# Kernel tuning notes

Hardware: AMD Instinct MI355X
Metric: run time of the kernel (lower is better)

Reference implementation:

```python
import jax, jax.numpy as jnp
import numpy as np

EPS = 1e-5
K = 20


def knn_idx(x, k):
    # x: (B, N, C) -> (B, N, k) indices of k nearest neighbors (incl. self)
    x2 = jnp.sum(x * x, axis=-1)                         # (B, N)
    inner = jnp.einsum('bnc,bmc->bnm', x, x)             # (B, N, N)
    neg_dist = 2.0 * inner - x2[:, :, None] - x2[:, None, :]
    _, idx = jax.lax.top_k(neg_dist, k)                  # (B, N, k)
    return idx


def graph_feature(x, idx):
    # x: (B, N, C), idx: (B, N, k) -> (B, N, k, 2C) = cat([x_j - x_i, x_i])
    nbr = jax.vmap(lambda xb, ib: xb[ib])(x, idx)        # (B, N, k, C)
    xi = jnp.broadcast_to(x[:, :, None, :], nbr.shape)
    return jnp.concatenate([nbr - xi, xi], axis=-1)


def bn_lrelu(x, gamma, beta):
    # eval-mode BatchNorm (running_mean=0, running_var=1) + LeakyReLU(0.2)
    y = x * (gamma / jnp.sqrt(1.0 + EPS)) + beta
    return jnp.where(y >= 0, y, 0.2 * y)


def edge_conv(x, W, gamma, beta, k):
    # x: (B, N, C) -> (B, N, O); 1x1 conv over edge features + max over k
    idx = knn_idx(x, k)
    feat = graph_feature(x, idx)                         # (B, N, k, 2C)
    y = jnp.einsum('bnkc,oc->bnko', feat, W)
    y = bn_lrelu(y, gamma, beta)
    return jnp.max(y, axis=2)                            # (B, N, O)


def setup_inputs() -> dict:
    key = jax.random.key(0)
    ks = jax.random.split(key, 7)
    d = {
        'points': jax.random.normal(ks[0], (8, 2048, 3), dtype=jnp.float32),
        'W1': jax.random.normal(ks[1], (64, 6), dtype=jnp.float32) * 0.1,
        'W2': jax.random.normal(ks[2], (64, 128), dtype=jnp.float32) * 0.1,
        'W3': jax.random.normal(ks[3], (128, 128), dtype=jnp.float32) * 0.1,
        'W4': jax.random.normal(ks[4], (256, 256), dtype=jnp.float32) * 0.1,
        'W5': jax.random.normal(ks[5], (1024, 512), dtype=jnp.float32) * 0.1,
    }
    for name, c in [('1', 64), ('2', 64), ('3', 128), ('4', 256), ('5', 1024)]:
        d['g' + name] = jnp.ones((c,), dtype=jnp.float32)
        d['b' + name] = jnp.zeros((c,), dtype=jnp.float32)
    return d


def reference(points, W1, W2, W3, W4, W5, g1, g2, g3, g4, g5, b1, b2, b3, b4, b5):
    x1 = edge_conv(points, W1, g1, b1, K)                # (B, N, 64)
    x2 = edge_conv(x1, W2, g2, b2, K)                    # (B, N, 64)
    x3 = edge_conv(x2, W3, g3, b3, K)                    # (B, N, 128)
    x4 = edge_conv(x3, W4, g4, b4, K)                    # (B, N, 256)
    x_cat = jnp.concatenate([x1, x2, x3, x4], axis=-1)   # (B, N, 512)
    feat = bn_lrelu(jnp.einsum('bnc,oc->bno', x_cat, W5), g5, b5)  # (B, N, 1024)
    max_pool = jnp.max(feat, axis=1)
    avg_pool = jnp.mean(feat, axis=1)
    return jnp.concatenate([max_pool, avg_pool], axis=-1)  # (B, 2048)
```

## Files before the change

### kernel.cpp

```cpp
#include <hip/hip_runtime.h>
#include <math.h>

#define BATCH 8
#define NPTS 2048
#define KNN 20
#define BN_TOTAL (BATCH * NPTS)
#define EPSV 1e-5f

__global__ __launch_bounds__(256) void x2_kernel(const float* __restrict__ x, int C, int ldx,
                                                 float* __restrict__ x2) {
    int i = blockIdx.x * 256 + threadIdx.x;
    if (i >= BN_TOTAL) return;
    const float* xr = x + (size_t)i * ldx;
    float s = 0.f;
    if ((ldx & 3) == 0 && (C & 3) == 0) {
        const float4* xr4 = (const float4*)xr;
        for (int c = 0; c < (C >> 2); ++c) {
            float4 v = xr4[c];
            s = fmaf(v.x, v.x, s); s = fmaf(v.y, v.y, s);
            s = fmaf(v.z, v.z, s); s = fmaf(v.w, v.w, s);
        }
    } else {
        for (int c = 0; c < C; ++c) s = fmaf(xr[c], xr[c], s);
    }
    x2[i] = s;
}

__global__ __launch_bounds__(256) void dist_kernel(const float* __restrict__ x,
                                                   const float* __restrict__ x2,
                                                   int C, int ldx, int b0,
                                                   float* __restrict__ S) {
    __shared__ float As[16][136];
    __shared__ float Bs[16][136];
    int z = blockIdx.z;
    int b = b0 + z;
    int i0 = blockIdx.x * 128, j0 = blockIdx.y * 128;
    const float* xb = x + (size_t)b * NPTS * ldx;
    int tid = threadIdx.x;
    int tm = tid >> 4, tn = tid & 15;

    float acc[8][8] = {};
    int KT = (C + 15) >> 4;
    for (int kt = 0; kt < KT; ++kt) {
        int k0 = kt << 4;
#pragma unroll
        for (int s = tid; s < 512; s += 256) {
            int r = s >> 2, c4 = s & 3;
            int kk = k0 + c4 * 4;
            float va[4], vb[4];
            if (kk + 3 < C && (ldx & 3) == 0) {
                float4 a = *(const float4*)&xb[(size_t)(i0 + r) * ldx + kk];
                float4 bv = *(const float4*)&xb[(size_t)(j0 + r) * ldx + kk];
                va[0] = a.x; va[1] = a.y; va[2] = a.z; va[3] = a.w;
                vb[0] = bv.x; vb[1] = bv.y; vb[2] = bv.z; vb[3] = bv.w;
            } else {
#pragma unroll
                for (int u = 0; u < 4; ++u) {
                    int k = kk + u;
                    va[u] = (k < C) ? xb[(size_t)(i0 + r) * ldx + k] : 0.f;
                    vb[u] = (k < C) ? xb[(size_t)(j0 + r) * ldx + k] : 0.f;
                }
            }
#pragma unroll
            for (int u = 0; u < 4; ++u) {
                As[c4 * 4 + u][r] = va[u];
                Bs[c4 * 4 + u][r] = vb[u];
            }
        }
        __syncthreads();
#pragma unroll
        for (int k = 0; k < 16; ++k) {
            float4 a0 = *(const float4*)&As[k][tm * 8];
            float4 a1 = *(const float4*)&As[k][tm * 8 + 4];
            float4 c0 = *(const float4*)&Bs[k][tn * 8];
            float4 c1 = *(const float4*)&Bs[k][tn * 8 + 4];
            float av[8] = {a0.x, a0.y, a0.z, a0.w, a1.x, a1.y, a1.z, a1.w};
            float bv[8] = {c0.x, c0.y, c0.z, c0.w, c1.x, c1.y, c1.z, c1.w};
#pragma unroll
            for (int mi = 0; mi < 8; ++mi)
#pragma unroll
                for (int ni = 0; ni < 8; ++ni)
                    acc[mi][ni] = fmaf(av[mi], bv[ni], acc[mi][ni]);
        }
        __syncthreads();
    }

    const float* x2b = x2 + (size_t)b * NPTS;
    float xj[8];
#pragma unroll
    for (int u = 0; u < 8; ++u) xj[u] = x2b[j0 + tn * 8 + u];
#pragma unroll
    for (int mi = 0; mi < 8; ++mi) {
        float xi = x2b[i0 + tm * 8 + mi];
        float4 o0, o1;
        o0.x = 2.f * acc[mi][0] - xi - xj[0];
        o0.y = 2.f * acc[mi][1] - xi - xj[1];
        o0.z = 2.f * acc[mi][2] - xi - xj[2];
        o0.w = 2.f * acc[mi][3] - xi - xj[3];
        o1.x = 2.f * acc[mi][4] - xi - xj[4];
        o1.y = 2.f * acc[mi][5] - xi - xj[5];
        o1.z = 2.f * acc[mi][6] - xi - xj[6];
        o1.w = 2.f * acc[mi][7] - xi - xj[7];
        size_t rowp = ((size_t)z * NPTS + i0 + tm * 8 + mi) * NPTS + j0 + tn * 8;
        *(float4*)&S[rowp] = o0;
        *(float4*)&S[rowp + 4] = o1;
    }
}

__global__ __launch_bounds__(256) void topk_kernel(const float* __restrict__ S, int b0,
                                                   int* __restrict__ idx_out) {
    int lane = threadIdx.x & 63, w = threadIdx.x >> 6;
    int row = blockIdx.x * 4 + w;
    const float4* S4 = (const float4*)(S + (size_t)row * NPTS);

    float v[32];
    float lm = -INFINITY; int li = 0;
#pragma unroll
    for (int r4 = 0; r4 < 8; ++r4) {
        float4 f = S4[lane * 8 + r4];
        v[r4 * 4 + 0] = f.x; v[r4 * 4 + 1] = f.y;
        v[r4 * 4 + 2] = f.z; v[r4 * 4 + 3] = f.w;
    }
#pragma unroll
    for (int q = 0; q < 32; ++q)
        if (v[q] > lm) { lm = v[q]; li = q; }

    int sel = 0;
    for (int it = 0; it < KNN; ++it) {
        float bv = lm;
        int bi = (lane << 5) | li;
#pragma unroll
        for (int d = 1; d < 64; d <<= 1) {
            float ov = __shfl_xor(bv, d);
            int oi = __shfl_xor(bi, d);
            if (ov > bv || (ov == bv && oi < bi)) { bv = ov; bi = oi; }
        }
        if (lane == it) sel = bi;
        if ((bi >> 5) == lane) {
            int r = bi & 31;
#pragma unroll
            for (int q = 0; q < 32; ++q)
                if (q == r) v[q] = -INFINITY;
            lm = -INFINITY; li = 0;
#pragma unroll
            for (int q = 0; q < 32; ++q)
                if (v[q] > lm) { lm = v[q]; li = q; }
        }
    }
    int z = row >> 11, i = row & 2047;
    int bn = (b0 + z) * NPTS + i;
    if (lane < KNN) idx_out[bn * KNN + lane] = sel;
}

__global__ __launch_bounds__(256) void pq_gemm(const float* __restrict__ X, int C, int ldx,
                                               const float* __restrict__ W, int O,
                                               float* __restrict__ PQ) {
    __shared__ float As[32][68];
    __shared__ float Bs[32][68];
    int i0 = blockIdx.x * 64, j0 = blockIdx.y * 64;
    int tid = threadIdx.x;
    int tm = tid >> 4, tn = tid & 15;
    int N2 = 2 * O;

    float acc[4][4] = {};
    int KT = (C + 31) >> 5;
    for (int kt = 0; kt < KT; ++kt) {
        int k0 = kt << 5;
        for (int e = tid; e < 2048; e += 256) {
            int m = e >> 5, k = e & 31;
            int kk = k0 + k;
            As[k][m] = (kk < C) ? X[(size_t)(i0 + m) * ldx + kk] : 0.f;
            int o = j0 + m;
            float wv = 0.f;
            if (kk < C)
                wv = (o < O) ? W[(size_t)o * 2 * C + kk] : W[(size_t)(o - O) * 2 * C + C + kk];
            Bs[k][m] = wv;
        }
        __syncthreads();
#pragma unroll
        for (int k = 0; k < 32; ++k) {
            float4 a = *(const float4*)&As[k][tm * 4];
            float4 bb = *(const float4*)&Bs[k][tn * 4];
            float av[4] = {a.x, a.y, a.z, a.w};
            float bv[4] = {bb.x, bb.y, bb.z, bb.w};
#pragma unroll
            for (int mi = 0; mi < 4; ++mi)
#pragma unroll
                for (int ni = 0; ni < 4; ++ni)
                    acc[mi][ni] = fmaf(av[mi], bv[ni], acc[mi][ni]);
        }
        __syncthreads();
    }
#pragma unroll
    for (int mi = 0; mi < 4; ++mi) {
        float4 o;
        o.x = acc[mi][0]; o.y = acc[mi][1]; o.z = acc[mi][2]; o.w = acc[mi][3];
        *(float4*)&PQ[(size_t)(i0 + tm * 4 + mi) * N2 + j0 + tn * 4] = o;
    }
}

__global__ __launch_bounds__(256) void gmax_kernel(const float* __restrict__ PQ,
                                                   const int* __restrict__ idx, int O, int oshift,
                                                   const float* __restrict__ gamma,
                                                   const float* __restrict__ beta,
                                                   float* __restrict__ out, int ldo) {
    __shared__ int s_idx[4][KNN];
    int rpb = 256 >> oshift;
    int lr = threadIdx.x >> oshift;
    int o = threadIdx.x & (O - 1);
    int bn = blockIdx.x * rpb + lr;
    int b = bn >> 11;
    if (o < KNN) s_idx[lr][o] = idx[bn * KNN + o];
    __syncthreads();
    const float inv = 1.0f / sqrtf(1.0f + EPSV);
    int N2 = 2 * O;
    size_t brow = (size_t)(b << 11);
    float mx = -INFINITY, mn = INFINITY;
#pragma unroll
    for (int k = 0; k < KNN; ++k) {
        float v = PQ[(brow + s_idx[lr][k]) * N2 + o];
        mx = fmaxf(mx, v);
        mn = fminf(mn, v);
    }
    float pn = PQ[(size_t)bn * N2 + o];
    float qn = PQ[(size_t)bn * N2 + O + o];
    float sc = gamma[o] * inv;
    float m = (sc >= 0.f) ? mx : mn;
    float z = sc * (m - pn + qn) + beta[o];
    out[(size_t)bn * ldo + o] = (z >= 0.f) ? z : 0.2f * z;
}

__global__ __launch_bounds__(256) void final_gemm(const float* __restrict__ xcat,
                                                  const float* __restrict__ W5,
                                                  const float* __restrict__ g5,
                                                  const float* __restrict__ b5,
                                                  float* __restrict__ part) {
    __shared__ float As[16][136];
    __shared__ float Bs[16][136];
    __shared__ float s_red[2][16][132];
    int i0 = blockIdx.x * 128;
    int j0 = blockIdx.y * 128;
    int tid = threadIdx.x;
    int tm = tid >> 4, tn = tid & 15;

    float acc[8][8] = {};
    for (int kt = 0; kt < 32; ++kt) {
        int k0 = kt << 4;
#pragma unroll
        for (int s = tid; s < 512; s += 256) {
            int r = s >> 2, c4 = s & 3;
            int kk = k0 + c4 * 4;
            float4 va = *(const float4*)&xcat[(size_t)(i0 + r) * 512 + kk];
            float4 vb = *(const float4*)&W5[(size_t)(j0 + r) * 512 + kk];
            As[c4 * 4 + 0][r] = va.x; As[c4 * 4 + 1][r] = va.y;
            As[c4 * 4 + 2][r] = va.z; As[c4 * 4 + 3][r] = va.w;
            Bs[c4 * 4 + 0][r] = vb.x; Bs[c4 * 4 + 1][r] = vb.y;
            Bs[c4 * 4 + 2][r] = vb.z; Bs[c4 * 4 + 3][r] = vb.w;
        }
        __syncthreads();
#pragma unroll
        for (int k = 0; k < 16; ++k) {
            float4 a0 = *(const float4*)&As[k][tm * 8];
            float4 a1 = *(const float4*)&As[k][tm * 8 + 4];
            float4 c0 = *(const float4*)&Bs[k][tn * 8];
            float4 c1 = *(const float4*)&Bs[k][tn * 8 + 4];
            float av[8] = {a0.x, a0.y, a0.z, a0.w, a1.x, a1.y, a1.z, a1.w};
            float bv[8] = {c0.x, c0.y, c0.z, c0.w, c1.x, c1.y, c1.z, c1.w};
#pragma unroll
            for (int mi = 0; mi < 8; ++mi)
#pragma unroll
                for (int ni = 0; ni < 8; ++ni)
                    acc[mi][ni] = fmaf(av[mi], bv[ni], acc[mi][ni]);
        }
        __syncthreads();
    }

    const float inv = 1.0f / sqrtf(1.0f + EPSV);
#pragma unroll
    for (int u = 0; u < 8; ++u) {
        int o = j0 + tn * 8 + u;
        float sc = g5[o] * inv;
        float bi = b5[o];
        float mx = -INFINITY, sm = 0.f;
#pragma unroll
        for (int mi = 0; mi < 8; ++mi) {
            float z = fmaf(sc, acc[mi][u], bi);
            z = (z >= 0.f) ? z : 0.2f * z;
            mx = fmaxf(mx, z);
            sm += z;
        }
        s_red[0][tm][tn * 8 + u] = mx;
        s_red[1][tm][tn * 8 + u] = sm;
    }
    __syncthreads();
    if (tid < 128) {
        int o = tid;
        float m = -INFINITY, s = 0.f;
#pragma unroll
        for (int t = 0; t < 16; ++t) {
            m = fmaxf(m, s_red[0][t][o]);
            s += s_red[1][t][o];
        }
        int b = i0 >> 11, nt = (i0 >> 7) & 15;
        size_t base = (size_t)((b * 16 + nt) * 2) * 1024 + j0 + o;
        part[base] = m;
        part[base + 1024] = s;
    }
}

__global__ __launch_bounds__(256) void freduce_kernel(const float* __restrict__ part,
                                                      float* __restrict__ out) {
    int t = blockIdx.x * 256 + threadIdx.x;
    if (t >= 8 * 1024) return;
    int b = t >> 10, o = t & 1023;
    float m = -INFINITY, s = 0.f;
#pragma unroll
    for (int nt = 0; nt < 16; ++nt) {
        size_t base = (size_t)((b * 16 + nt) * 2) * 1024 + o;
        m = fmaxf(m, part[base]);
        s += part[base + 1024];
    }
    out[b * 2048 + o] = m;
    out[b * 2048 + 1024 + o] = s * (1.0f / 2048.0f);
}

extern "C" void kernel_launch(void* const* d_in, const int* in_sizes, int n_in,
                              void* d_out, int out_size, void* d_ws, size_t ws_size,
                              hipStream_t stream) {
    const float* points = (const float*)d_in[0];
    const float* W1 = (const float*)d_in[1];
    const float* W2 = (const float*)d_in[2];
    const float* W3 = (const float*)d_in[3];
    const float* W4 = (const float*)d_in[4];
    const float* W5 = (const float*)d_in[5];
    const float* g1 = (const float*)d_in[6];
    const float* b1 = (const float*)d_in[7];
    const float* g2 = (const float*)d_in[8];
    const float* b2 = (const float*)d_in[9];
    const float* g3 = (const float*)d_in[10];
    const float* b3 = (const float*)d_in[11];
    const float* g4 = (const float*)d_in[12];
    const float* b4 = (const float*)d_in[13];
    const float* g5 = (const float*)d_in[14];
    const float* b5 = (const float*)d_in[15];
    float* out = (float*)d_out;

    const size_t f_xcat = (size_t)BN_TOTAL * 512;
    const size_t f_x2 = BN_TOTAL;
    const size_t f_idx = (size_t)BN_TOTAL * KNN;
    const size_t f_part = (size_t)8 * 16 * 2 * 1024;
    const size_t fixedf = f_xcat + f_x2 + f_idx + f_part;
    auto needB = [&](int c) {
        size_t spq = (size_t)c * NPTS * NPTS;
        if (spq < f_xcat) spq = f_xcat;
        return 4ull * (fixedf + spq);
    };
    int cB = 2;
    if (ws_size >= needB(8)) cB = 8;
    else if (ws_size >= needB(4)) cB = 4;
    size_t spq_f = (size_t)cB * NPTS * NPTS;
    if (spq_f < f_xcat) spq_f = f_xcat;

    float* xcat = (float*)d_ws;
    float* SPQ = xcat + f_xcat;
    float* x2 = SPQ + spq_f;
    int* idx = (int*)(x2 + f_x2);
    float* part = (float*)(idx + f_idx);

    auto layer = [&](const float* xin, int C, int ldx, const float* W, int O, int oshift,
                     const float* ga, const float* be, float* xout) {
        x2_kernel<<<(BN_TOTAL + 255) / 256, 256, 0, stream>>>(xin, C, ldx, x2);
        for (int b0 = 0; b0 < BATCH; b0 += cB) {
            dist_kernel<<<dim3(16, 16, cB), 256, 0, stream>>>(xin, x2, C, ldx, b0, SPQ);
            topk_kernel<<<cB * 512, 256, 0, stream>>>(SPQ, b0, idx);
        }
        pq_gemm<<<dim3(BN_TOTAL / 64, (2 * O) / 64), 256, 0, stream>>>(xin, C, ldx, W, O, SPQ);
        int rpb = 256 >> oshift;
        gmax_kernel<<<BN_TOTAL / rpb, 256, 0, stream>>>(SPQ, idx, O, oshift, ga, be, xout, 512);
    };

    layer(points,     3,   3,   W1, 64,  6, g1, b1, xcat + 0);
    layer(xcat + 0,   64,  512, W2, 64,  6, g2, b2, xcat + 64);
    layer(xcat + 64,  64,  512, W3, 128, 7, g3, b3, xcat + 128);
    layer(xcat + 128, 128, 512, W4, 256, 8, g4, b4, xcat + 256);

    final_gemm<<<dim3(BN_TOTAL / 128, 1024 / 128), 256, 0, stream>>>(xcat, W5, g5, b5, part);
    freduce_kernel<<<(8 * 1024 + 255) / 256, 256, 0, stream>>>(part, out);
}
```

Baseline: 1.109 ms.

## Run final GEMM on bf16 MFMA with hi/lo split for fp32-like accuracy

Replaces the scalar-FMA final 512->1024 GEMM with a matrix-core kernel using bf16 16x16x32 MFMA. Accuracy is kept near fp32 through a three-term hi/lo split (hi*hi + hi*lo + lo*hi). Operands are pre-split into bf16 hi/lo buffers by new conversion kernels. LDS uses an XOR swizzle and the next tile is prefetched into registers. It also shrinks the dist_kernel LDS padding, and adds extra workspace, two launches and conversion traffic.

```diff
diff --git a/kernel.cpp b/kernel.cpp
--- a/kernel.cpp
+++ b/kernel.cpp
@@ -6,6 +6,9 @@
 #define KNN 20
 #define BN_TOTAL (BATCH * NPTS)
 #define EPSV 1e-5f
+
+typedef __attribute__((ext_vector_type(8))) short short8v;
+typedef __attribute__((ext_vector_type(4))) float floatx4;
 
 __global__ __launch_bounds__(256) void x2_kernel(const float* __restrict__ x, int C, int ldx,
                                                  float* __restrict__ x2) {
@@ -30,8 +33,8 @@
                                                    const float* __restrict__ x2,
                                                    int C, int ldx, int b0,
                                                    float* __restrict__ S) {
-    __shared__ float As[16][136];
-    __shared__ float Bs[16][136];
+    __shared__ float As[16][132];
+    __shared__ float Bs[16][132];
     int z = blockIdx.z;
     int b = b0 + z;
     int i0 = blockIdx.x * 128, j0 = blockIdx.y * 128;
@@ -230,79 +233,137 @@
     out[(size_t)bn * ldo + o] = (z >= 0.f) ? z : 0.2f * z;
 }
 
-__global__ __launch_bounds__(256) void final_gemm(const float* __restrict__ xcat,
-                                                  const float* __restrict__ W5,
+__device__ __forceinline__ unsigned short bf16_rne(float x) {
+    union { float f; unsigned u; } cv; cv.f = x;
+    unsigned r = (cv.u + 0x7fffu + ((cv.u >> 16) & 1u)) >> 16;
+    return (unsigned short)r;
+}
+__global__ __launch_bounds__(256) void split_bf16_kernel(const float* __restrict__ in, int n4,
+                                                         unsigned short* __restrict__ hi,
+                                                         unsigned short* __restrict__ lo) {
+    int i = blockIdx.x * 256 + threadIdx.x;
+    if (i >= n4) return;
+    float4 v = ((const float4*)in)[i];
+    float vv[4] = {v.x, v.y, v.z, v.w};
+    ushort4 h, l;
+    unsigned short hh[4], ll[4];
+#pragma unroll
+    for (int u = 0; u < 4; ++u) {
+        unsigned short hb = bf16_rne(vv[u]);
+        union { unsigned u32; float f; } hf; hf.u32 = ((unsigned)hb) << 16;
+        hh[u] = hb;
+        ll[u] = bf16_rne(vv[u] - hf.f);
+    }
+    h.x = hh[0]; h.y = hh[1]; h.z = hh[2]; h.w = hh[3];
+    l.x = ll[0]; l.y = ll[1]; l.z = ll[2]; l.w = ll[3];
+    *(ushort4*)(hi + (size_t)i * 4) = h;
+    *(ushort4*)(lo + (size_t)i * 4) = l;
+}
+
+__global__ __launch_bounds__(256) void final_mfma(const unsigned short* __restrict__ Xhi,
+                                                  const unsigned short* __restrict__ Xlo,
+                                                  const unsigned short* __restrict__ Whi,
+                                                  const unsigned short* __restrict__ Wlo,
                                                   const float* __restrict__ g5,
                                                   const float* __restrict__ b5,
                                                   float* __restrict__ part) {
-    __shared__ float As[16][136];
-    __shared__ float Bs[16][136];
-    __shared__ float s_red[2][16][132];
+    __shared__ __align__(16) char As[128 * 64];
+    __shared__ __align__(16) char Bs[128 * 64];
+    __shared__ float sredM[2][128];
+    __shared__ float sredS[2][128];
+
+    int tid = threadIdx.x;
     int i0 = blockIdx.x * 128;
     int j0 = blockIdx.y * 128;
-    int tid = threadIdx.x;
-    int tm = tid >> 4, tn = tid & 15;
-
-    float acc[8][8] = {};
-    for (int kt = 0; kt < 32; ++kt) {
-        int k0 = kt << 4;
-#pragma unroll
-        for (int s = tid; s < 512; s += 256) {
-            int r = s >> 2, c4 = s & 3;
-            int kk = k0 + c4 * 4;
-            float4 va = *(const float4*)&xcat[(size_t)(i0 + r) * 512 + kk];
-            float4 vb = *(const float4*)&W5[(size_t)(j0 + r) * 512 + kk];
-            As[c4 * 4 + 0][r] = va.x; As[c4 * 4 + 1][r] = va.y;
-            As[c4 * 4 + 2][r] = va.z; As[c4 * 4 + 3][r] = va.w;
-            Bs[c4 * 4 + 0][r] = vb.x; Bs[c4 * 4 + 1][r] = vb.y;
-            Bs[c4 * 4 + 2][r] = vb.z; Bs[c4 * 4 + 3][r] = vb.w;
-        }
-        __syncthreads();
-#pragma unroll
-        for (int k = 0; k < 16; ++k) {
-            float4 a0 = *(const float4*)&As[k][tm * 8];
-            float4 a1 = *(const float4*)&As[k][tm * 8 + 4];
-            float4 c0 = *(const float4*)&Bs[k][tn * 8];
-            float4 c1 = *(const float4*)&Bs[k][tn * 8 + 4];
-            float av[8] = {a0.x, a0.y, a0.z, a0.w, a1.x, a1.y, a1.z, a1.w};
-            float bv[8] = {c0.x, c0.y, c0.z, c0.w, c1.x, c1.y, c1.z, c1.w};
-#pragma unroll
-            for (int mi = 0; mi < 8; ++mi)
-#pragma unroll
-                for (int ni = 0; ni < 8; ++ni)
-                    acc[mi][ni] = fmaf(av[mi], bv[ni], acc[mi][ni]);
-        }
-        __syncthreads();
+    int lane = tid & 63, w = tid >> 6;
+    int wr = w >> 1, wc = w & 1;
+
+    int rowA = tid >> 2, q = tid & 3;
+    auto swz = [](int row, int qq) { return (row * 64 + qq * 16) ^ ((row & 7) << 4); };
+    int wa0 = swz(rowA, q), wa1 = swz(rowA + 64, q);
+
+    int fr = lane & 15, slot = lane >> 4;
+    int aoff[4], boff[4];
+#pragma unroll
+    for (int m = 0; m < 4; ++m) {
+        int ra = wr * 64 + m * 16 + fr;
+        aoff[m] = (ra * 64 + slot * 16) ^ ((ra & 7) << 4);
+        int rb = wc * 64 + m * 16 + fr;
+        boff[m] = (rb * 64 + slot * 16) ^ ((rb & 7) << 4);
+    }
+
+    floatx4 acc[4][4];
+#pragma unroll
+    for (int m = 0; m < 4; ++m)
+#pragma unroll
+        for (int n = 0; n < 4; ++n)
+            acc[m][n] = (floatx4){0.f, 0.f, 0.f, 0.f};
+
+    uint4 ra0, ra1, rb0, rb1;
+    auto prefetch = [&](int it) {
+        int seg = it >> 4;
+        int kk = (it & 15) * 32;
+        const unsigned short* Ab = ((seg < 2) ? Xhi : Xlo) + (size_t)i0 * 512 + kk + q * 8;
+        const unsigned short* Bb = ((seg == 1) ? Wlo : Whi) + (size_t)j0 * 512 + kk + q * 8;
+        ra0 = *(const uint4*)(Ab + (size_t)rowA * 512);
+        ra1 = *(const uint4*)(Ab + (size_t)(rowA + 64) * 512);
+        rb0 = *(const uint4*)(Bb + (size_t)rowA * 512);
+        rb1 = *(const uint4*)(Bb + (size_t)(rowA + 64) * 512);
+    };
+
+    prefetch(0);
+    for (int it = 0; it < 48; ++it) {
+        __syncthreads();
+        *(uint4*)(As + wa0) = ra0;
+        *(uint4*)(As + wa1) = ra1;
+        *(uint4*)(Bs + wa0) = rb0;
+        *(uint4*)(Bs + wa1) = rb1;
+        __syncthreads();
+        if (it < 47) prefetch(it + 1);
+        short8v af[4], bf[4];
+#pragma unroll
+        for (int m = 0; m < 4; ++m) af[m] = *(const short8v*)(As + aoff[m]);
+#pragma unroll
+        for (int n = 0; n < 4; ++n) bf[n] = *(const short8v*)(Bs + boff[n]);
+#pragma unroll
+        for (int m = 0; m < 4; ++m)
+#pragma unroll
+            for (int n = 0; n < 4; ++n)
+                acc[m][n] = __builtin_amdgcn_mfma_f32_16x16x32_bf16(af[m], bf[n], acc[m][n], 0, 0, 0);
     }
 
     const float inv = 1.0f / sqrtf(1.0f + EPSV);
 #pragma unroll
-    for (int u = 0; u < 8; ++u) {
-        int o = j0 + tn * 8 + u;
+    for (int n = 0; n < 4; ++n) {
+        int o = j0 + wc * 64 + n * 16 + fr;
         float sc = g5[o] * inv;
         float bi = b5[o];
         float mx = -INFINITY, sm = 0.f;
 #pragma unroll
-        for (int mi = 0; mi < 8; ++mi) {
-            float z = fmaf(sc, acc[mi][u], bi);
-            z = (z >= 0.f) ? z : 0.2f * z;
-            mx = fmaxf(mx, z);
-            sm += z;
-        }
-        s_red[0][tm][tn * 8 + u] = mx;
-        s_red[1][tm][tn * 8 + u] = sm;
+        for (int m = 0; m < 4; ++m)
+#pragma unroll
+            for (int r = 0; r < 4; ++r) {
+                float z = fmaf(sc, acc[m][n][r], bi);
+                z = (z >= 0.f) ? z : 0.2f * z;
+                mx = fmaxf(mx, z);
+                sm += z;
+            }
+#pragma unroll
+        for (int d = 16; d < 64; d <<= 1) {
+            mx = fmaxf(mx, __shfl_xor(mx, d));
+            sm += __shfl_xor(sm, d);
+        }
+        if (slot == 0) {
+            sredM[wr][wc * 64 + n * 16 + fr] = mx;
+            sredS[wr][wc * 64 + n * 16 + fr] = sm;
+        }
     }
     __syncthreads();
     if (tid < 128) {
-        int o = tid;
-        float m = -INFINITY, s = 0.f;
-#pragma unroll
-        for (int t = 0; t < 16; ++t) {
-            m = fmaxf(m, s_red[0][t][o]);
-            s += s_red[1][t][o];
-        }
+        float m = fmaxf(sredM[0][tid], sredM[1][tid]);
+        float s = sredS[0][tid] + sredS[1][tid];
         int b = i0 >> 11, nt = (i0 >> 7) & 15;
-        size_t base = (size_t)((b * 16 + nt) * 2) * 1024 + j0 + o;
+        size_t base = (size_t)((b * 16 + nt) * 2) * 1024 + j0 + tid;
         part[base] = m;
         part[base + 1024] = s;
     }
@@ -346,10 +407,12 @@
     float* out = (float*)d_out;
 
     const size_t f_xcat = (size_t)BN_TOTAL * 512;
+    const size_t f_w5 = (size_t)1024 * 512;
     const size_t f_x2 = BN_TOTAL;
     const size_t f_idx = (size_t)BN_TOTAL * KNN;
     const size_t f_part = (size_t)8 * 16 * 2 * 1024;
-    const size_t fixedf = f_xcat + f_x2 + f_idx + f_part;
+    const size_t f_bf16 = f_xcat + f_w5;
+    const size_t fixedf = f_xcat + f_x2 + f_idx + f_part + f_bf16;
     auto needB = [&](int c) {
         size_t spq = (size_t)c * NPTS * NPTS;
         if (spq < f_xcat) spq = f_xcat;
@@ -366,6 +429,10 @@
     float* x2 = SPQ + spq_f;
     int* idx = (int*)(x2 + f_x2);
     float* part = (float*)(idx + f_idx);
+    unsigned short* Xhi = (unsigned short*)(part + f_part);
+    unsigned short* Xlo = Xhi + f_xcat;
+    unsigned short* Whi = Xlo + f_xcat;
+    unsigned short* Wlo = Whi + f_w5;
 
     auto layer = [&](const float* xin, int C, int ldx, const float* W, int O, int oshift,
                      const float* ga, const float* be, float* xout) {
@@ -384,6 +451,8 @@
     layer(xcat + 64,  64,  512, W3, 128, 7, g3, b3, xcat + 128);
     layer(xcat + 128, 128, 512, W4, 256, 8, g4, b4, xcat + 256);
 
-    final_gemm<<<dim3(BN_TOTAL / 128, 1024 / 128), 256, 0, stream>>>(xcat, W5, g5, b5, part);
+    split_bf16_kernel<<<(int)((f_xcat / 4 + 255) / 256), 256, 0, stream>>>(xcat, (int)(f_xcat / 4), Xhi, Xlo);
+    split_bf16_kernel<<<(int)((f_w5 / 4 + 255) / 256), 256, 0, stream>>>(W5, (int)(f_w5 / 4), Whi, Wlo);
+    final_mfma<<<dim3(BN_TOTAL / 128, 1024 / 128), 256, 0, stream>>>(Xhi, Xlo, Whi, Wlo, g5, b5, part);
     freduce_kernel<<<(8 * 1024 + 255) / 256, 256, 0, stream>>>(part, out);
 }
```

After: 966.1 us. 12.9% less time.
